# Optimization experiments

Measured on AMD Instinct MI355X. Metric: run time of the kernel, lower is better.

## Reference

```python
import jax, jax.numpy as jnp
import numpy as np

N_BINS = 64
SIGMA_SCALE = 0.5
_LAB_RANGES = {'L': (0.0, 100.0), 'a': (-128.0, 127.0), 'b': (-128.0, 127.0)}


def _channel_params(vmin, vmax, n_bins=N_BINS, sigma_scale=SIGMA_SCALE):
    delta = (vmax - vmin) / n_bins
    centers = jnp.linspace(vmin + delta / 2, vmax - delta / 2, n_bins, dtype=jnp.float32)
    sigma = jnp.float32(delta * sigma_scale)
    return centers, sigma


def rgb_to_lab(rgb):
    # rgb: (B, 3, H, W) in [0, 1] sRGB
    thr = 0.04045
    lin = jnp.where(rgb > thr, jnp.power((rgb + 0.055) / 1.055, 2.4), rgb / 12.92)
    r, g, b = lin[:, 0], lin[:, 1], lin[:, 2]
    # sRGB -> XYZ (D65)
    x = 0.412453 * r + 0.357580 * g + 0.180423 * b
    y = 0.212671 * r + 0.715160 * g + 0.072169 * b
    z = 0.019334 * r + 0.119193 * g + 0.950227 * b
    xn, zn = 0.950456, 1.088754  # D65 white (Y normalized to 1)
    x = x / xn
    z = z / zn
    eps = 0.008856
    def f(t):
        return jnp.where(t > eps, jnp.cbrt(t), 7.787 * t + 16.0 / 116.0)
    fx, fy, fz = f(x), f(y), f(z)
    L = 116.0 * fy - 16.0
    a = 500.0 * (fx - fy)
    bb = 200.0 * (fy - fz)
    return jnp.stack([L, a, bb], axis=1)  # (B, 3, H, W)


def setup_inputs() -> dict:
    key = jax.random.key(0)
    img = jax.random.uniform(key, (16, 3, 512, 512), dtype=jnp.float32)
    return {"img": img}


def reference(img) -> jnp.ndarray:
    B = img.shape[0]
    img_lab = rgb_to_lab(img)  # (B, 3, H, W)
    parts = []
    for c_idx, name in enumerate(['L', 'a', 'b']):
        centers, sigma = _channel_params(*_LAB_RANGES[name])
        pixels = img_lab[:, c_idx].reshape(B, -1)  # (B, HW)
        diff = pixels[:, :, None] - centers[None, None, :]  # (B, HW, n_bins)
        weights = jnp.exp(-(diff ** 2) / (2.0 * sigma ** 2))
        hist_unnorm = weights.sum(axis=1)  # (B, n_bins)
        hist = hist_unnorm / (hist_unnorm.sum(axis=-1, keepdims=True) + 1e-8)
        parts.append(hist)
    return jnp.concatenate(parts, axis=1)  # (B, 192)
```

## Files before the change

### kernel.cpp

```cpp
#include <hip/hip_runtime.h>
#include <cmath>

#define HW (512*512)
#define NSUB 2048
#define THREADS1 1024
#define BLKS_PER_IMG 32

__global__ __launch_bounds__(THREADS1) void count_kernel(const float* __restrict__ img,
                                                         unsigned* __restrict__ part) {
    __shared__ unsigned sh[2][3 * NSUB];
    const int tid = threadIdx.x;
    unsigned* flat = &sh[0][0];
    for (int i = tid; i < 2 * 3 * NSUB; i += THREADS1) flat[i] = 0u;
    __syncthreads();

    unsigned* h = sh[(tid >> 6) & 1];

    const int b  = blockIdx.y;
    const int bx = blockIdx.x;
    const float* base = img + (size_t)b * 3u * HW;

    const int stride = BLKS_PER_IMG * THREADS1 * 4;
    for (int p = (bx * THREADS1 + tid) * 4; p < HW; p += stride) {
        float4 r4 = *reinterpret_cast<const float4*>(base + p);
        float4 g4 = *reinterpret_cast<const float4*>(base + p + HW);
        float4 b4 = *reinterpret_cast<const float4*>(base + p + 2 * HW);
        float rr[4] = {r4.x, r4.y, r4.z, r4.w};
        float gg[4] = {g4.x, g4.y, g4.z, g4.w};
        float bl[4] = {b4.x, b4.y, b4.z, b4.w};

        #pragma unroll
        for (int k = 0; k < 4; ++k) {
            float lr = (rr[k] > 0.04045f) ? exp2f(2.4f * log2f((rr[k] + 0.055f) * (1.0f / 1.055f))) : rr[k] * (1.0f / 12.92f);
            float lg = (gg[k] > 0.04045f) ? exp2f(2.4f * log2f((gg[k] + 0.055f) * (1.0f / 1.055f))) : gg[k] * (1.0f / 12.92f);
            float lb = (bl[k] > 0.04045f) ? exp2f(2.4f * log2f((bl[k] + 0.055f) * (1.0f / 1.055f))) : bl[k] * (1.0f / 12.92f);

            float x = 0.4339530f * lr + 0.3762197f * lg + 0.1898288f * lb;
            float y = 0.2126710f * lr + 0.7151600f * lg + 0.0721690f * lb;
            float z = 0.0177578f * lr + 0.1094766f * lg + 0.8727661f * lb;

            float fx = (x > 0.008856f) ? exp2f(log2f(x) * (1.0f/3.0f)) : 7.787f * x + 16.0f/116.0f;
            float fy = (y > 0.008856f) ? exp2f(log2f(y) * (1.0f/3.0f)) : 7.787f * y + 16.0f/116.0f;
            float fz = (z > 0.008856f) ? exp2f(log2f(z) * (1.0f/3.0f)) : 7.787f * z + 16.0f/116.0f;

            int iL = (int)(2375.68f    * fy - 327.68f);
            int iA = (int)(4015.6863f  * (fx - fy) + 1028.01569f);
            int iB = (int)(1606.27451f * (fy - fz) + 1028.01569f);

            atomicAdd(&h[iL], 1u);
            atomicAdd(&h[NSUB + iA], 1u);
            atomicAdd(&h[2 * NSUB + iB], 1u);
        }
    }
    __syncthreads();

    unsigned* dst = part + ((size_t)(b * BLKS_PER_IMG + bx)) * 3 * NSUB;
    for (int i = tid; i < 3 * NSUB; i += THREADS1) dst[i] = sh[0][i] + sh[1][i];
}

__global__ __launch_bounds__(256) void conv_norm_kernel(const unsigned* __restrict__ part,
                                                        float* __restrict__ out) {
    __shared__ float sub[NSUB];
    __shared__ float hb[64];
    const int img = blockIdx.x / 3;
    const int ch  = blockIdx.x % 3;
    const int t   = threadIdx.x;

    const unsigned* p0 = part + (size_t)img * BLKS_PER_IMG * 3 * NSUB + (size_t)ch * NSUB;
    float acc8[8] = {0,0,0,0,0,0,0,0};
    for (int k = 0; k < BLKS_PER_IMG; ++k) {
        const unsigned* pk = p0 + (size_t)k * 3 * NSUB + t * 8;
        uint4 a = *reinterpret_cast<const uint4*>(pk);
        uint4 c = *reinterpret_cast<const uint4*>(pk + 4);
        acc8[0] += (float)a.x; acc8[1] += (float)a.y;
        acc8[2] += (float)a.z; acc8[3] += (float)a.w;
        acc8[4] += (float)c.x; acc8[5] += (float)c.y;
        acc8[6] += (float)c.z; acc8[7] += (float)c.w;
    }
    #pragma unroll
    for (int i = 0; i < 8; ++i) sub[t * 8 + i] = acc8[i];
    __syncthreads();

    const int j = t >> 2;
    const int q = t & 3;
    const float C = 2.8853901f;
    const float jf = (float)j + 0.5f - (0.5f / 32.0f);
    const int s_lo = 32 * j - 86;
    float acc = 0.0f;
    for (int i = 0; i < 51; ++i) {
        int ii = i + j; if (ii >= 51) ii -= 51;
        int s  = s_lo + q + 4 * ii;
        if ((unsigned)s < (unsigned)NSUB) {
            float d = (float)s * (1.0f / 32.0f) - jf;
            acc += sub[s] * exp2f(-C * d * d);
        }
    }
    acc += __shfl_xor(acc, 1, 64);
    acc += __shfl_xor(acc, 2, 64);
    if (q == 0) hb[j] = acc;
    __syncthreads();

    if (t < 64) {
        float v = hb[t];
        float s = v;
        #pragma unroll
        for (int off = 32; off >= 1; off >>= 1) s += __shfl_down(s, off, 64);
        s = __shfl(s, 0, 64);
        out[img * 192 + ch * 64 + t] = v / (s + 1e-8f);
    }
}

extern "C" void kernel_launch(void* const* d_in, const int* in_sizes, int n_in,
                              void* d_out, int out_size, void* d_ws, size_t ws_size,
                              hipStream_t stream) {
    const float* img = (const float*)d_in[0];
    float* out     = (float*)d_out;
    unsigned* part = (unsigned*)d_ws;

    const int B = in_sizes[0] / (3 * HW);

    count_kernel<<<dim3(BLKS_PER_IMG, B), THREADS1, 0, stream>>>(img, part);
    conv_norm_kernel<<<B * 3, 256, 0, stream>>>(part, out);
}
```

Baseline: 97.31 us.

## Pack partial histograms to 16-bit, use hardware exp2/log2, widen conv kernel

Count kernel now uses raw hardware exp2/log intrinsics instead of the accurate libm versions, cutting transcendental cost in the colour conversion. Partial sub-bin counts are packed two per 32-bit word, halving the partial-histogram write and read traffic. The conv/normalize kernel runs 1024 threads per block, with 16 lanes per output bin and a shorter unrolled loop. Risks: packed counts overflow if a single block's sub-bin count exceeds 65535, and the intrinsics carry slightly lower precision.

```diff
diff --git a/kernel.cpp b/kernel.cpp
--- a/kernel.cpp
+++ b/kernel.cpp
@@ -5,6 +5,10 @@
 #define NSUB 2048
 #define THREADS1 1024
 #define BLKS_PER_IMG 32
+#define PART_WORDS (3 * NSUB / 2)
+
+__device__ __forceinline__ float fexp2(float x) { return __builtin_amdgcn_exp2f(x); }
+__device__ __forceinline__ float flog2(float x) { return __builtin_amdgcn_logf(x); }
 
 __global__ __launch_bounds__(THREADS1) void count_kernel(const float* __restrict__ img,
                                                          unsigned* __restrict__ part) {
@@ -31,17 +35,17 @@
 
         #pragma unroll
         for (int k = 0; k < 4; ++k) {
-            float lr = (rr[k] > 0.04045f) ? exp2f(2.4f * log2f((rr[k] + 0.055f) * (1.0f / 1.055f))) : rr[k] * (1.0f / 12.92f);
-            float lg = (gg[k] > 0.04045f) ? exp2f(2.4f * log2f((gg[k] + 0.055f) * (1.0f / 1.055f))) : gg[k] * (1.0f / 12.92f);
-            float lb = (bl[k] > 0.04045f) ? exp2f(2.4f * log2f((bl[k] + 0.055f) * (1.0f / 1.055f))) : bl[k] * (1.0f / 12.92f);
+            float lr = (rr[k] > 0.04045f) ? fexp2(2.4f * flog2((rr[k] + 0.055f) * (1.0f / 1.055f))) : rr[k] * (1.0f / 12.92f);
+            float lg = (gg[k] > 0.04045f) ? fexp2(2.4f * flog2((gg[k] + 0.055f) * (1.0f / 1.055f))) : gg[k] * (1.0f / 12.92f);
+            float lb = (bl[k] > 0.04045f) ? fexp2(2.4f * flog2((bl[k] + 0.055f) * (1.0f / 1.055f))) : bl[k] * (1.0f / 12.92f);
 
             float x = 0.4339530f * lr + 0.3762197f * lg + 0.1898288f * lb;
             float y = 0.2126710f * lr + 0.7151600f * lg + 0.0721690f * lb;
             float z = 0.0177578f * lr + 0.1094766f * lg + 0.8727661f * lb;
 
-            float fx = (x > 0.008856f) ? exp2f(log2f(x) * (1.0f/3.0f)) : 7.787f * x + 16.0f/116.0f;
-            float fy = (y > 0.008856f) ? exp2f(log2f(y) * (1.0f/3.0f)) : 7.787f * y + 16.0f/116.0f;
-            float fz = (z > 0.008856f) ? exp2f(log2f(z) * (1.0f/3.0f)) : 7.787f * z + 16.0f/116.0f;
+            float fx = (x > 0.008856f) ? fexp2(flog2(x) * (1.0f/3.0f)) : 7.787f * x + 16.0f/116.0f;
+            float fy = (y > 0.008856f) ? fexp2(flog2(y) * (1.0f/3.0f)) : 7.787f * y + 16.0f/116.0f;
+            float fz = (z > 0.008856f) ? fexp2(flog2(z) * (1.0f/3.0f)) : 7.787f * z + 16.0f/116.0f;
 
             int iL = (int)(2375.68f    * fy - 327.68f);
             int iA = (int)(4015.6863f  * (fx - fy) + 1028.01569f);
@@ -54,49 +58,53 @@
     }
     __syncthreads();
 
-    unsigned* dst = part + ((size_t)(b * BLKS_PER_IMG + bx)) * 3 * NSUB;
-    for (int i = tid; i < 3 * NSUB; i += THREADS1) dst[i] = sh[0][i] + sh[1][i];
+    unsigned* dst = part + (size_t)(b * BLKS_PER_IMG + bx) * PART_WORDS;
+    for (int i = tid; i < PART_WORDS; i += THREADS1) {
+        unsigned s0 = sh[0][2 * i]     + sh[1][2 * i];
+        unsigned s1 = sh[0][2 * i + 1] + sh[1][2 * i + 1];
+        dst[i] = s0 | (s1 << 16);
+    }
 }
 
-__global__ __launch_bounds__(256) void conv_norm_kernel(const unsigned* __restrict__ part,
-                                                        float* __restrict__ out) {
+__global__ __launch_bounds__(1024) void conv_norm_kernel(const unsigned* __restrict__ part,
+                                                         float* __restrict__ out) {
     __shared__ float sub[NSUB];
     __shared__ float hb[64];
     const int img = blockIdx.x / 3;
     const int ch  = blockIdx.x % 3;
     const int t   = threadIdx.x;
 
-    const unsigned* p0 = part + (size_t)img * BLKS_PER_IMG * 3 * NSUB + (size_t)ch * NSUB;
-    float acc8[8] = {0,0,0,0,0,0,0,0};
+    const unsigned* p0 = part + (size_t)img * BLKS_PER_IMG * PART_WORDS
+                              + (size_t)ch * (NSUB / 2) + t;
+    unsigned s0 = 0, s1 = 0;
+    #pragma unroll
     for (int k = 0; k < BLKS_PER_IMG; ++k) {
-        const unsigned* pk = p0 + (size_t)k * 3 * NSUB + t * 8;
-        uint4 a = *reinterpret_cast<const uint4*>(pk);
-        uint4 c = *reinterpret_cast<const uint4*>(pk + 4);
-        acc8[0] += (float)a.x; acc8[1] += (float)a.y;
-        acc8[2] += (float)a.z; acc8[3] += (float)a.w;
-        acc8[4] += (float)c.x; acc8[5] += (float)c.y;
-        acc8[6] += (float)c.z; acc8[7] += (float)c.w;
+        unsigned v = p0[(size_t)k * PART_WORDS];
+        s0 += v & 0xFFFFu;
+        s1 += v >> 16;
     }
-    #pragma unroll
-    for (int i = 0; i < 8; ++i) sub[t * 8 + i] = acc8[i];
+    sub[2 * t]     = (float)s0;
+    sub[2 * t + 1] = (float)s1;
     __syncthreads();
 
-    const int j = t >> 2;
-    const int q = t & 3;
+    const int j = t >> 4;
+    const int q = t & 15;
     const float C = 2.8853901f;
     const float jf = (float)j + 0.5f - (0.5f / 32.0f);
     const int s_lo = 32 * j - 86;
     float acc = 0.0f;
-    for (int i = 0; i < 51; ++i) {
-        int ii = i + j; if (ii >= 51) ii -= 51;
-        int s  = s_lo + q + 4 * ii;
-        if ((unsigned)s < (unsigned)NSUB) {
+    #pragma unroll
+    for (int i = 0; i < 13; ++i) {
+        int s = s_lo + q + 16 * i;
+        if (s < s_lo + 204 && (unsigned)s < (unsigned)NSUB) {
             float d = (float)s * (1.0f / 32.0f) - jf;
-            acc += sub[s] * exp2f(-C * d * d);
+            acc += sub[s] * fexp2(-C * d * d);
         }
     }
     acc += __shfl_xor(acc, 1, 64);
     acc += __shfl_xor(acc, 2, 64);
+    acc += __shfl_xor(acc, 4, 64);
+    acc += __shfl_xor(acc, 8, 64);
     if (q == 0) hb[j] = acc;
     __syncthreads();
 
@@ -120,5 +128,5 @@
     const int B = in_sizes[0] / (3 * HW);
 
     count_kernel<<<dim3(BLKS_PER_IMG, B), THREADS1, 0, stream>>>(img, part);
-    conv_norm_kernel<<<B * 3, 256, 0, stream>>>(part, out);
+    conv_norm_kernel<<<B * 3, 1024, 0, stream>>>(part, out);
 }
```

After: 87.19 us. 10.4% less time.
